# Optimization experiments

Measured on AMD Instinct MI355X. Metric: run time of the kernel, lower is better.

Reference implementation:

```python
import jax, jax.numpy as jnp
import numpy as np

IN_C, HID, N_NODES, WINDOW = 8, 64, 20000, 8
N_BIG = N_NODES * WINDOW          # 160000 supernodes (window-stacked graph)
E, E_DEC = 1_600_000, 500_000
EPS = 1e-5
DH = 2 * HID + IN_C + WINDOW - 1  # 143, decoder hidden size


def _gcn(x, row, col, ew, W, b, n):
    # GCNConv with self-loops + symmetric normalization (PyG semantics)
    loop = jnp.arange(n)
    r = jnp.concatenate([row, loop])
    c = jnp.concatenate([col, loop])
    w = jnp.concatenate([ew, jnp.ones((n,), ew.dtype)])
    deg = jax.ops.segment_sum(w, c, num_segments=n)
    dis = jnp.where(deg > 0, jax.lax.rsqrt(jnp.maximum(deg, EPS)), 0.0)
    norm = dis[r] * w * dis[c]
    h = x @ W                                  # [n, HID]
    agg = jax.ops.segment_sum(norm[:, None] * h[r], c, num_segments=n)
    return agg + b


def _bn(x, g, be):
    # BatchNorm1d, training-mode batch statistics (biased var)
    m = x.mean(0)
    v = x.var(0)
    return (x - m) * jax.lax.rsqrt(v + EPS) * g + be


def _lstm(X, Wih, Whh, bih, bhh):
    # X: [T, B, F]; PyTorch gate order i,f,g,o
    Hd = Whh.shape[1]
    B = X.shape[1]

    def step(carry, xt):
        h, c = carry
        gates = xt @ Wih.T + h @ Whh.T + bih + bhh
        i, f, g, o = jnp.split(gates, 4, axis=-1)
        c = jax.nn.sigmoid(f) * c + jax.nn.sigmoid(i) * jnp.tanh(g)
        h = jax.nn.sigmoid(o) * jnp.tanh(c)
        return (h, c), h

    init = (jnp.zeros((B, Hd), X.dtype), jnp.zeros((B, Hd), X.dtype))
    (h, _), ys = jax.lax.scan(step, init, X)
    return ys, h


def setup_inputs() -> dict:
    key = jax.random.key(0)
    ks = jax.random.split(key, 20)
    f32 = jnp.float32
    sc = lambda k, shape, fan: (jax.random.normal(k, shape, f32) / np.sqrt(fan)).astype(f32)
    d = {}
    d["x"] = jax.random.normal(ks[0], (N_BIG, IN_C), f32)
    d["edge_attr"] = jax.random.uniform(ks[1], (E,), f32)
    d["edge_index"] = jax.random.randint(ks[2], (2, E), 0, N_BIG)
    d["edge_weights_index"] = jax.random.randint(ks[3], (2, E_DEC), 0, N_NODES)
    # GCN layer 1 and 2
    d["W1"] = sc(ks[4], (IN_C, HID), IN_C); d["b1"] = jnp.zeros((HID,), f32)
    d["g1"] = jnp.ones((HID,), f32); d["be1"] = jnp.zeros((HID,), f32)
    d["W2"] = sc(ks[5], (HID, HID), HID); d["b2"] = jnp.zeros((HID,), f32)
    d["g2"] = jnp.ones((HID,), f32); d["be2"] = jnp.zeros((HID,), f32)
    # LSTM 1 (input 2*HID) and LSTM 2 (input HID)
    d["Wih1"] = sc(ks[6], (4 * HID, 2 * HID), 2 * HID)
    d["Whh1"] = sc(ks[7], (4 * HID, HID), HID)
    d["bih1"] = jnp.zeros((4 * HID,), f32); d["bhh1"] = jnp.zeros((4 * HID,), f32)
    d["Wih2"] = sc(ks[8], (4 * HID, HID), HID)
    d["Whh2"] = sc(ks[9], (4 * HID, HID), HID)
    d["bih2"] = jnp.zeros((4 * HID,), f32); d["bhh2"] = jnp.zeros((4 * HID,), f32)
    # Edge decoder MLP
    d["dWa"] = sc(ks[10], (2 * DH, DH), 2 * DH); d["dba"] = jnp.zeros((DH,), f32)
    d["dWb"] = sc(ks[11], (DH, 1), DH); d["dbb"] = jnp.zeros((1,), f32)
    return d


def reference(x, edge_attr, W1, b1, g1, be1, W2, b2, g2, be2,
              Wih1, Whh1, bih1, bhh1, Wih2, Whh2, bih2, bhh2,
              dWa, dba, dWb, dbb, edge_index, edge_weights_index):
    row, col = edge_index[0], edge_index[1]
    # skip features S: first timestep full features + last channel of later steps
    Sx = x.reshape(WINDOW, N_NODES, IN_C).transpose(1, 0, 2)   # [N, W, C]
    S = jnp.concatenate([Sx[:, 0, :], Sx[:, 1:, IN_C - 1]], axis=1)  # [N, C+W-1]
    # two GCN layers (relu -> batchnorm; dropout identity in eval)
    h1 = _bn(jax.nn.relu(_gcn(x, row, col, edge_attr, W1, b1, N_BIG)), g1, be1)
    h2 = _bn(jax.nn.relu(_gcn(h1, row, col, edge_attr, W2, b2, N_BIG)), g2, be2)
    Xc = jnp.concatenate([h1, h2], axis=1).reshape(WINDOW, N_NODES, 2 * HID)
    y1, H1 = _lstm(Xc, Wih1, Whh1, bih1, bhh1)
    _, H2 = _lstm(y1, Wih2, Whh2, bih2, bhh2)
    node_emb = jnp.concatenate([H1, H2, S], axis=1)  # [N_NODES, DH]
    # edge decoder: gather-concat-MLP
    src, trg = edge_weights_index[0], edge_weights_index[1]
    ee = jnp.concatenate([node_emb[src], node_emb[trg]], axis=1)  # [E_DEC, 2*DH]
    h = jax.nn.relu(ee @ dWa + dba)
    return (h @ dWb + dbb).reshape(-1)
```

## Files before the change

kernel.cpp:

```cpp
#include <hip/hip_runtime.h>
#include <hip/hip_bf16.h>

#define IN_C 8
#define HID 64
#define N_NODES 20000
#define WINDOW 8
#define N_BIG 160000
#define NE 1600000
#define E_DEC 500000
#define DHV 143
#define EPSV 1e-5f
#define CAP 32
#define OVF_CAP 4096
#define NER 168
#define QS 16384.0f
#define IQS (1.0f / 16384.0f)
#define NPART 8
#define PART_SZ (N_BIG / NPART)
#define NEB (NE / 256)

typedef __hip_bfloat16 bf;
typedef __attribute__((ext_vector_type(8))) short short8;
typedef __attribute__((ext_vector_type(4))) float float4_;

__device__ __forceinline__ float b2f(bf v) { return __bfloat162float(v); }
__device__ __forceinline__ bf f2b(float v) { return __float2bfloat16(v); }
__device__ __forceinline__ float bflo(unsigned int u) { return __uint_as_float(u << 16); }
__device__ __forceinline__ float bfhi(unsigned int u) { return __uint_as_float(u & 0xffff0000u); }
__device__ __forceinline__ unsigned int packbf2(float lo, float hi) {
    unsigned int ul = __bfloat16_as_ushort(f2b(lo));
    unsigned int uh = __bfloat16_as_ushort(f2b(hi));
    return ul | (uh << 16);
}
__device__ __forceinline__ float sigf(float x) {
    return __builtin_amdgcn_rcpf(1.f + __expf(-x));
}
__device__ __forceinline__ float tanhfast(float x) {
    x = fminf(fmaxf(x, -15.f), 15.f);
    float e = __expf(2.f * x);
    return (e - 1.f) * __builtin_amdgcn_rcpf(e + 1.f);
}

__global__ __launch_bounds__(256) void k_prepfill(
    const int* ei, const float* ea, int* cnt, unsigned int* bucket, int* ovfn, float4* ovf,
    const float* Wih2, const float* Whh2, const float* bih1, const float* bhh1,
    const float* bih2, const float* bhh2, const float* dWa,
    bf* B2f, float* bc1, float* bc2, bf* Bpqf)
{
    int tid = threadIdx.x;
    if (blockIdx.x < NPART * NEB) {
        int p = blockIdx.x & (NPART - 1);
        int chunk = blockIdx.x >> 3;
        int e = chunk * 256 + tid;
        int c = ei[NE + e];
        if (c >= p * PART_SZ && c < (p + 1) * PART_SZ) {
            int r = ei[e];
            float a = ea[e];
            unsigned int q = (unsigned int)(a * QS + 0.5f);
            if (q > 16383u) q = 16383u;
            int pp = atomicAdd(&cnt[c], 1);
            if (pp < CAP) bucket[(size_t)c * CAP + pp] = ((unsigned int)r << 14) | q;
            else {
                int qq = atomicAdd(ovfn, 1);
                if (qq < OVF_CAP) ovf[qq] = make_float4(__int_as_float(c), __int_as_float(r), a, 0.f);
            }
        }
        return;
    }
    int i0 = (blockIdx.x - NPART * NEB) * 256 + tid;
    int stride = 512 * 256;
    for (int i = i0; i < 16 * 4 * 64 * 8; i += stride) {
        int j = i & 7, lane = (i >> 3) & 63, r = i >> 9;
        int c = r & 3, ct = r >> 2;
        int q = lane >> 4, l15 = lane & 15;
        int n = ct * 16 + l15, k = c * 32 + q * 8 + j;
        B2f[i] = f2b((k < 64) ? Wih2[n * 64 + k] : Whh2[n * 64 + (k - 64)]);
    }
    for (int i = i0; i < 256; i += stride) {
        bc1[i] = bih1[i] + bhh1[i];
        bc2[i] = bih2[i] + bhh2[i];
    }
    for (int i = i0; i < 18 * 5 * 64 * 8; i += stride) {
        int j = i & 7, lane = (i >> 3) & 63, r = i >> 9;
        int c = r % 5, ct = r / 5;
        int q = lane >> 4, l15 = lane & 15;
        int n = ct * 16 + l15, k = c * 32 + q * 8 + j;
        float v = 0.f;
        if (k < DHV) {
            if (n < DHV) v = dWa[k * DHV + n];
            else if (n >= 144 && n < 144 + DHV) v = dWa[(DHV + k) * DHV + (n - 144)];
        }
        Bpqf[i] = f2b(v);
    }
}

__global__ __launch_bounds__(256) void k_xw1dis(const float* x, const float* W1,
        const int* cnt, const unsigned int* bucket, const int* ovfn, const float4* ovf,
        float* dis, bf* hbufb) {
    __shared__ float Ws[8][64];
    __shared__ float xs[8][8];
    int tid = threadIdx.x;
    Ws[tid >> 6][tid & 63] = W1[tid];
    Ws[4 + (tid >> 6)][tid & 63] = W1[256 + tid];
    int nb0 = blockIdx.x * 8;
    if (tid < 64) xs[tid >> 3][tid & 7] = x[nb0 * IN_C + tid];
    __syncthreads();
    int wv = tid >> 6, half = (tid >> 5) & 1, l = tid & 31;
    int nl = wv * 2 + half;
    int c = nb0 + nl;
    int n = cnt[c];
    int nbk = (n < CAP) ? n : CAP;
    float s = 0.f;
    for (int i = l; i < nbk; i += 32) s += (float)(bucket[(size_t)c * CAP + i] & 0x3FFFu);
    s *= IQS;
    if (n > CAP) {
        int m = *ovfn; if (m > OVF_CAP) m = OVF_CAP;
        for (int i = l; i < m; i += 32) {
            float4 v = ovf[i];
            if (__float_as_int(v.x) == c) s += v.z;
        }
    }
#pragma unroll
    for (int off = 16; off > 0; off >>= 1) s += __shfl_xor(s, off);
    float dv = rsqrtf(fmaxf(1.f + s, EPSV));
    if (l == 0) dis[c] = dv;
    float a0 = 0.f, a1 = 0.f;
#pragma unroll
    for (int k = 0; k < IN_C; k++) {
        float xv = xs[nl][k];
        a0 += xv * Ws[k][2 * l];
        a1 += xv * Ws[k][2 * l + 1];
    }
    *(unsigned int*)(hbufb + (size_t)c * 64 + 2 * l) = packbf2(dv * a0, dv * a1);
}

__global__ __launch_bounds__(256) void k_gcn_gather(const bf* h, const float* dis, const int* cnt,
                             const unsigned int* bucket, const int* ovfn, const float4* ovf,
                             const float* bias, bf* outb, float* part) {
    __shared__ float4 red[256];
    int tid = threadIdx.x;
    int wv = (blockIdx.x * 256 + tid) >> 6;
    int half = (tid >> 5) & 1, l = tid & 31;
    int c = wv * 2 + half;
    unsigned int hv = *(const unsigned int*)(h + (size_t)c * 64 + 2 * l);
    float ax = bflo(hv), ay = bfhi(hv);
    size_t o = (size_t)c * CAP;
    int nfull = cnt[c];
    int n = (nfull < CAP) ? nfull : CAP;
    int e = 0;
    for (; e + 8 <= n; e += 8) {
        unsigned int p[8];
#pragma unroll
        for (int j = 0; j < 8; j++) p[j] = bucket[o + e + j];
        unsigned int v[8];
#pragma unroll
        for (int j = 0; j < 8; j++)
            v[j] = *(const unsigned int*)(h + (size_t)(p[j] >> 14) * 64 + 2 * l);
#pragma unroll
        for (int j = 0; j < 8; j++) {
            float a = (float)(p[j] & 0x3FFFu) * IQS;
            ax += a * bflo(v[j]); ay += a * bfhi(v[j]);
        }
    }
    for (; e + 4 <= n; e += 4) {
        unsigned int p[4];
#pragma unroll
        for (int j = 0; j < 4; j++) p[j] = bucket[o + e + j];
        unsigned int v[4];
#pragma unroll
        for (int j = 0; j < 4; j++)
            v[j] = *(const unsigned int*)(h + (size_t)(p[j] >> 14) * 64 + 2 * l);
#pragma unroll
        for (int j = 0; j < 4; j++) {
            float a = (float)(p[j] & 0x3FFFu) * IQS;
            ax += a * bflo(v[j]); ay += a * bfhi(v[j]);
        }
    }
    for (; e < n; e++) {
        unsigned int p = bucket[o + e];
        unsigned int v = *(const unsigned int*)(h + (size_t)(p >> 14) * 64 + 2 * l);
        float a = (float)(p & 0x3FFFu) * IQS;
        ax += a * bflo(v);
        ay += a * bfhi(v);
    }
    if (nfull > CAP) {
        int m = *ovfn; if (m > OVF_CAP) m = OVF_CAP;
        for (int i = 0; i < m; i++) {
            float4 v = ovf[i];
            if (__float_as_int(v.x) == c) {
                unsigned int hw = *(const unsigned int*)(h + (size_t)__float_as_int(v.y) * 64 + 2 * l);
                ax += v.z * bflo(hw);
                ay += v.z * bfhi(hw);
            }
        }
    }
    float dv = dis[c];
    float2 bv = *(const float2*)(bias + 2 * l);
    float vx = fmaxf(dv * ax + bv.x, 0.f);
    float vy = fmaxf(dv * ay + bv.y, 0.f);
    *(unsigned int*)(outb + (size_t)c * 64 + 2 * l) = packbf2(vx, vy);
    red[tid] = make_float4(vx, vy, vx * vx, vy * vy);
    __syncthreads();
    if (tid < 32) {
        float4 s = make_float4(0.f, 0.f, 0.f, 0.f);
#pragma unroll
        for (int i = 0; i < 8; i++) {
            float4 v = red[((i >> 1) << 6) + ((i & 1) << 5) + tid];
            s.x += v.x; s.y += v.y; s.z += v.z; s.w += v.w;
        }
        float* pb = part + (size_t)blockIdx.x * 128;
        pb[2 * tid] = s.x; pb[2 * tid + 1] = s.y;
        pb[64 + 2 * tid] = s.z; pb[64 + 2 * tid + 1] = s.w;
    }
}

__global__ __launch_bounds__(256) void k_bnred(const float* part, int nblk, float* stats_out) {
    __shared__ float s[256];
    float acc = 0.f;
    for (int b = threadIdx.x; b < nblk; b += 256) acc += part[(size_t)b * 128 + blockIdx.x];
    s[threadIdx.x] = acc;
    __syncthreads();
    for (int off = 128; off; off >>= 1) {
        if (threadIdx.x < off) s[threadIdx.x] += s[threadIdx.x + off];
        __syncthreads();
    }
    if (threadIdx.x == 0) stats_out[blockIdx.x] = s[0];
}

__global__ __launch_bounds__(256) void k_fold1(const float* W2, const float* g1, const float* be1,
                                               const float* stats, bf* W2t, float* w2b, float* AC) {
    __shared__ float A[64], C[64];
    int tid = threadIdx.x;
    if (tid < 64) {
        float m = stats[tid] * (1.f / (float)N_BIG);
        float var = stats[64 + tid] * (1.f / (float)N_BIG) - m * m;
        float a = g1[tid] * rsqrtf(var + EPSV);
        float c = be1[tid] - m * a;
        A[tid] = a; C[tid] = c;
        AC[tid] = a; AC[64 + tid] = c;
    }
    __syncthreads();
    for (int i = tid; i < 4096; i += 256) {
        int n = i >> 6, k = i & 63;
        W2t[i] = f2b(W2[k * 64 + n] * A[k]);
    }
    if (tid < 64) {
        float s = 0.f;
        for (int k = 0; k < 64; k++) s += C[k] * W2[k * 64 + tid];
        w2b[tid] = s;
    }
}

__global__ void k_fold2(const float* Wih1, const float* Whh1,
                        const float* g2, const float* be2, const float* stats,
                        const float* AC, const float* bih1, const float* bhh1,
                        bf* B1f, float* bc1f) {
    int i0 = blockIdx.x * blockDim.x + threadIdx.x;
    int stride = gridDim.x * blockDim.x;
    for (int i = i0; i < 16 * 6 * 64 * 8; i += stride) {
        int j = i & 7, lane = (i >> 3) & 63, r = i >> 9;
        int c = r % 6, ct = r / 6;
        int q = lane >> 4, l15 = lane & 15;
        int n = ct * 16 + l15, k = c * 32 + q * 8 + j;
        float w = (k < 128) ? Wih1[n * 128 + k] : Whh1[n * 64 + (k - 128)];
        float scale = 1.f;
        if (k < 64) scale = AC[k];
        else if (k < 128) {
            int ch = k - 64;
            float m = stats[128 + ch] * (1.f / (float)N_BIG);
            float var = stats[192 + ch] * (1.f / (float)N_BIG) - m * m;
            scale = g2[ch] * rsqrtf(var + EPSV);
        }
        B1f[i] = f2b(w * scale);
    }
    for (int n = i0; n < 256; n += stride) {
        float s = bih1[n] + bhh1[n];
        for (int k = 0; k < 64; k++) s += AC[64 + k] * Wih1[n * 128 + k];
        for (int ch = 0; ch < 64; ch++) {
            float m = stats[128 + ch] * (1.f / (float)N_BIG);
            float var = stats[192 + ch] * (1.f / (float)N_BIG) - m * m;
            float a = g2[ch] * rsqrtf(var + EPSV);
            float c2v = be2[ch] - m * a;
            s += c2v * Wih1[n * 128 + 64 + ch];
        }
        bc1f[n] = s;
    }
}

__global__ __launch_bounds__(256) void k_h1w2(const bf* h1b, const bf* W2t, const float* w2b,
                                              const float* dis, bf* outb) {
    int tid = threadIdx.x, w = tid >> 6, lane = tid & 63;
    int q = lane >> 4, l15 = lane & 15;
    size_t r0 = (size_t)blockIdx.x * 64 + w * 16;
    float4_ acc[4];
#pragma unroll
    for (int ct = 0; ct < 4; ct++) acc[ct] = (float4_){0.f, 0.f, 0.f, 0.f};
#pragma unroll
    for (int c = 0; c < 2; c++) {
        int koff = c * 32 + q * 8;
        short8 a = *(const short8*)(h1b + (r0 + l15) * 64 + koff);
#pragma unroll
        for (int ct = 0; ct < 4; ct++) {
            short8 b = *(const short8*)(W2t + (size_t)(ct * 16 + l15) * 64 + koff);
            acc[ct] = __builtin_amdgcn_mfma_f32_16x16x32_bf16(a, b, acc[ct], 0, 0, 0);
        }
    }
    size_t node0 = r0 + q * 4;
#pragma unroll
    for (int reg = 0; reg < 4; reg++) {
        float dv = dis[node0 + reg];
#pragma unroll
        for (int ct = 0; ct < 4; ct++)
            outb[(node0 + reg) * 64 + ct * 16 + l15] = f2b(dv * (acc[ct][reg] + w2b[ct * 16 + l15]));
    }
}

__global__ __launch_bounds__(256, 1) void k_lstm_fused(
    const bf* h1b, const bf* h2b, const bf* B1f, const bf* B2f,
    const float* bc1, const float* bc2, bf* H1out, bf* H2out)
{
    __shared__ bf h1s[2][32][72];
    __shared__ bf h2s[2][32][72];
    int tid = threadIdx.x, w = tid >> 6, lane = tid & 63;
    int q = lane >> 4, l15 = lane & 15;
    int gnode0 = blockIdx.x * 32;
    short8 B1r[6][4];
    short8 B2r[4][4];
#pragma unroll
    for (int c = 0; c < 6; c++)
#pragma unroll
        for (int g = 0; g < 4; g++)
            B1r[c][g] = *(const short8*)(B1f + (size_t)(((w + 4 * g) * 6 + c) * 64 + lane) * 8);
#pragma unroll
    for (int c = 0; c < 4; c++)
#pragma unroll
        for (int g = 0; g < 4; g++)
            B2r[c][g] = *(const short8*)(B2f + (size_t)(((w + 4 * g) * 4 + c) * 64 + lane) * 8);
    float c1[2][4] = {}, c2[2][4] = {};
    float bv1[4], bv2[4];
#pragma unroll
    for (int g = 0; g < 4; g++) {
        bv1[g] = bc1[(w + 4 * g) * 16 + l15];
        bv2[g] = bc2[(w + 4 * g) * 16 + l15];
    }
    for (int t = 0; t < WINDOW; t++) {
        int cur = t & 1, prv = cur ^ 1;
        const size_t toff = (size_t)t * N_NODES * 64;
        float4_ acc[2][4];
#pragma unroll
        for (int m = 0; m < 2; m++)
#pragma unroll
            for (int g = 0; g < 4; g++) acc[m][g] = (float4_){bv1[g], bv1[g], bv1[g], bv1[g]};
#pragma unroll
        for (int c = 0; c < 4; c++) {
            const bf* sp = (c < 2) ? h1b + toff : h2b + toff;
            int koff = (c & 1) * 32 + q * 8;
#pragma unroll
            for (int m = 0; m < 2; m++) {
                short8 a = *(const short8*)(sp + (size_t)(gnode0 + m * 16 + l15) * 64 + koff);
#pragma unroll
                for (int g = 0; g < 4; g++)
                    acc[m][g] = __builtin_amdgcn_mfma_f32_16x16x32_bf16(a, B1r[c][g], acc[m][g], 0, 0, 0);
            }
        }
        if (t > 0) {
#pragma unroll
            for (int c = 4; c < 6; c++) {
                int koff = (c & 1) * 32 + q * 8;
#pragma unroll
                for (int m = 0; m < 2; m++) {
                    short8 a = *(const short8*)&h1s[prv][m * 16 + l15][koff];
#pragma unroll
                    for (int g = 0; g < 4; g++)
                        acc[m][g] = __builtin_amdgcn_mfma_f32_16x16x32_bf16(a, B1r[c][g], acc[m][g], 0, 0, 0);
                }
            }
        }
#pragma unroll
        for (int m = 0; m < 2; m++)
#pragma unroll
            for (int reg = 0; reg < 4; reg++) {
                float gi = acc[m][0][reg], gf = acc[m][1][reg];
                float gg = acc[m][2][reg], go = acc[m][3][reg];
                float co = (t == 0) ? 0.f : c1[m][reg];
                float cn = sigf(gf) * co + sigf(gi) * tanhfast(gg);
                float hn = sigf(go) * tanhfast(cn);
                c1[m][reg] = cn;
                int nl = m * 16 + q * 4 + reg;
                h1s[cur][nl][w * 16 + l15] = f2b(hn);
                if (t == WINDOW - 1)
                    H1out[(size_t)(gnode0 + nl) * 64 + w * 16 + l15] = f2b(hn);
            }
        __syncthreads();
#pragma unroll
        for (int m = 0; m < 2; m++)
#pragma unroll
            for (int g = 0; g < 4; g++) acc[m][g] = (float4_){bv2[g], bv2[g], bv2[g], bv2[g]};
#pragma unroll
        for (int c = 0; c < 2; c++) {
            int koff = (c & 1) * 32 + q * 8;
#pragma unroll
            for (int m = 0; m < 2; m++) {
                short8 a = *(const short8*)&h1s[cur][m * 16 + l15][koff];
#pragma unroll
                for (int g = 0; g < 4; g++)
                    acc[m][g] = __builtin_amdgcn_mfma_f32_16x16x32_bf16(a, B2r[c][g], acc[m][g], 0, 0, 0);
            }
        }
        if (t > 0) {
#pragma unroll
            for (int c = 2; c < 4; c++) {
                int koff = (c & 1) * 32 + q * 8;
#pragma unroll
                for (int m = 0; m < 2; m++) {
                    short8 a = *(const short8*)&h2s[prv][m * 16 + l15][koff];
#pragma unroll
                    for (int g = 0; g < 4; g++)
                        acc[m][g] = __builtin_amdgcn_mfma_f32_16x16x32_bf16(a, B2r[c][g], acc[m][g], 0, 0, 0);
                }
            }
        }
#pragma unroll
        for (int m = 0; m < 2; m++)
#pragma unroll
            for (int reg = 0; reg < 4; reg++) {
                float gi = acc[m][0][reg], gf = acc[m][1][reg];
                float gg = acc[m][2][reg], go = acc[m][3][reg];
                float co = (t == 0) ? 0.f : c2[m][reg];
                float cn = sigf(gf) * co + sigf(gi) * tanhfast(gg);
                float hn = sigf(go) * tanhfast(cn);
                c2[m][reg] = cn;
                int nl = m * 16 + q * 4 + reg;
                h2s[cur][nl][w * 16 + l15] = f2b(hn);
                if (t == WINDOW - 1)
                    H2out[(size_t)(gnode0 + nl) * 64 + w * 16 + l15] = f2b(hn);
            }
        __syncthreads();
    }
}

__global__ __launch_bounds__(256) void k_pq(const bf* H1, const bf* H2, const float* x,
                                            const bf* Bpqf, const float* dba, bf* PQb) {
    __shared__ bf ne[64][NER];
    int tid = threadIdx.x, w = tid >> 6, lane = tid & 63;
    int q = lane >> 4, l15 = lane & 15;
    int r0 = blockIdx.x * 64;
    for (int i = tid; i < 64 * 16; i += 256) {
        int rr = i >> 4, cc = (i & 15) * 4;
        int gr = r0 + rr;
        uint2 v1 = make_uint2(0u, 0u), v2 = make_uint2(0u, 0u);
        if (gr < N_NODES) {
            v1 = *(const uint2*)(H1 + (size_t)gr * 64 + cc);
            v2 = *(const uint2*)(H2 + (size_t)gr * 64 + cc);
        }
        *(uint2*)&ne[rr][cc] = v1;
        *(uint2*)&ne[rr][64 + cc] = v2;
    }
    for (int i = tid; i < 64 * 32; i += 256) {
        int rr = i >> 5, cc = 128 + (i & 31);
        int gr = r0 + rr;
        float v = 0.f;
        if (gr < N_NODES && cc < DHV) {
            int s = cc - 128;
            v = (s < 8) ? x[gr * IN_C + s] : x[(size_t)((s - 7) * N_NODES + gr) * IN_C + 7];
        }
        ne[rr][cc] = f2b(v);
    }
    __syncthreads();
    float4_ acc[18];
#pragma unroll
    for (int ct = 0; ct < 18; ct++) acc[ct] = (float4_){0.f, 0.f, 0.f, 0.f};
#pragma unroll
    for (int c = 0; c < 5; c++) {
        short8 a = *(const short8*)&ne[w * 16 + l15][c * 32 + q * 8];
#pragma unroll
        for (int ct = 0; ct < 18; ct++) {
            short8 b = *(const short8*)(Bpqf + (size_t)((ct * 5 + c) * 64 + lane) * 8);
            acc[ct] = __builtin_amdgcn_mfma_f32_16x16x32_bf16(a, b, acc[ct], 0, 0, 0);
        }
    }
#pragma unroll
    for (int reg = 0; reg < 4; reg++) {
        int nrow = r0 + w * 16 + q * 4 + reg;
        if (nrow < N_NODES)
#pragma unroll
            for (int ct = 0; ct < 18; ct++) {
                int col = ct * 16 + l15;
                float add = (ct < 9 && col < DHV) ? dba[col] : 0.f;
                PQb[(size_t)nrow * 288 + col] = f2b(acc[ct][reg] + add);
            }
    }
}

__global__ __launch_bounds__(256) void k_edge(const int* ewi, const bf* PQb,
                                              const float* dWb, const float* dbb, float* out) {
    int wv = (blockIdx.x * blockDim.x + threadIdx.x) >> 6;
    int half = (threadIdx.x >> 5) & 1, l = threadIdx.x & 31;
    int e = wv * 2 + half;
    if (e >= E_DEC) return;
    int src = ewi[e], trg = ewi[E_DEC + e];
    const bf* Pr = PQb + (size_t)src * 288;
    const bf* Qr = PQb + (size_t)trg * 288 + 144;
    float acc;
    {
        uint2 pv = *(const uint2*)(Pr + 4 * l);
        uint2 qv = *(const uint2*)(Qr + 4 * l);
        float4 wv4 = *(const float4*)(dWb + 4 * l);
        float s0 = fmaxf(bflo(pv.x) + bflo(qv.x), 0.f);
        float s1 = fmaxf(bfhi(pv.x) + bfhi(qv.x), 0.f);
        float s2 = fmaxf(bflo(pv.y) + bflo(qv.y), 0.f);
        float s3 = fmaxf(bfhi(pv.y) + bfhi(qv.y), 0.f);
        acc = s0 * wv4.x + s1 * wv4.y + s2 * wv4.z + s3 * wv4.w;
    }
    if (l < 4) {
        int u0 = 128 + 4 * l;
        uint2 pv = *(const uint2*)(Pr + u0);
        uint2 qv = *(const uint2*)(Qr + u0);
        float w0 = dWb[u0], w1 = dWb[u0 + 1], w2 = dWb[u0 + 2];
        float w3 = (u0 + 3 < DHV) ? dWb[u0 + 3] : 0.f;
        acc += fmaxf(bflo(pv.x) + bflo(qv.x), 0.f) * w0;
        acc += fmaxf(bfhi(pv.x) + bfhi(qv.x), 0.f) * w1;
        acc += fmaxf(bflo(pv.y) + bflo(qv.y), 0.f) * w2;
        acc += fmaxf(bfhi(pv.y) + bfhi(qv.y), 0.f) * w3;
    }
#pragma unroll
    for (int off = 16; off > 0; off >>= 1) acc += __shfl_xor(acc, off);
    if (l == 0) out[e] = acc + dbb[0];
}

extern "C" void kernel_launch(void* const* d_in, const int* in_sizes, int n_in,
                              void* d_out, int out_size, void* d_ws, size_t ws_size,
                              hipStream_t stream) {
    (void)in_sizes; (void)n_in; (void)out_size; (void)ws_size;
    const float* x    = (const float*)d_in[0];
    const float* ea   = (const float*)d_in[1];
    const int*   ei   = (const int*)d_in[2];
    const int*   ewi  = (const int*)d_in[3];
    const float* W1   = (const float*)d_in[4];
    const float* b1   = (const float*)d_in[5];
    const float* g1   = (const float*)d_in[6];
    const float* be1  = (const float*)d_in[7];
    const float* W2   = (const float*)d_in[8];
    const float* b2   = (const float*)d_in[9];
    const float* g2   = (const float*)d_in[10];
    const float* be2  = (const float*)d_in[11];
    const float* Wih1 = (const float*)d_in[12];
    const float* Whh1 = (const float*)d_in[13];
    const float* bih1 = (const float*)d_in[14];
    const float* bhh1 = (const float*)d_in[15];
    const float* Wih2 = (const float*)d_in[16];
    const float* Whh2 = (const float*)d_in[17];
    const float* bih2 = (const float*)d_in[18];
    const float* bhh2 = (const float*)d_in[19];
    const float* dWa  = (const float*)d_in[20];
    const float* dba  = (const float*)d_in[21];
    const float* dWb  = (const float*)d_in[22];
    const float* dbb  = (const float*)d_in[23];
    float* out = (float*)d_out;

    const size_t NSB = (size_t)N_BIG * 64;
    const size_t NS  = (size_t)N_NODES * 64;
    char* base = (char*)d_ws;
    size_t o = 0;
    float* dis  = (float*)(base + o); o += (size_t)N_BIG * 4;
    bf* PQb     = (bf*)(base + o);    o += NSB * 2;
    bf* hbufb   = (bf*)(base + o);    o += NSB * 2;
    bf* h1b     = (bf*)(base + o);    o += NSB * 2;
    bf* h2b     = (bf*)(base + o);    o += NSB * 2;
    bf* hs1     = (bf*)(base + o);    o += NS * 2;
    bf* hs2     = (bf*)(base + o);    o += NS * 2;
    bf* B1f     = (bf*)(base + o);    o += (size_t)16 * 6 * 64 * 8 * 2;
    bf* B2f     = (bf*)(base + o);    o += (size_t)16 * 4 * 64 * 8 * 2;
    bf* W2t     = (bf*)(base + o);    o += 64 * 64 * 2;
    bf* Bpqf    = (bf*)(base + o);    o += (size_t)18 * 5 * 64 * 8 * 2;
    float* bc1  = (float*)(base + o); o += 256 * 4;
    float* bc2  = (float*)(base + o); o += 256 * 4;
    float* stats= (float*)(base + o); o += 256 * 4;
    float* w2b  = (float*)(base + o); o += 64 * 4;
    float* AC   = (float*)(base + o); o += 128 * 4;
    float* bc1f = (float*)(base + o); o += 256 * 4;
    int* cnt    = (int*)(base + o);   o += (size_t)N_BIG * 4;
    int* ovfn   = (int*)(base + o);   o += 256 * 4;
    float4* ovf = (float4*)(base + o); o += (size_t)OVF_CAP * 16;
    unsigned int* bucket = (unsigned int*)(base + o); o += (size_t)N_BIG * CAP * 4;
    float* part = (float*)(base + o); o += (size_t)20000 * 128 * 4;

    hipMemsetAsync(cnt, 0, ((size_t)N_BIG + 256) * 4, stream);
    k_prepfill<<<NPART * NEB + 512, 256, 0, stream>>>(ei, ea, cnt, bucket, ovfn, ovf,
                                               Wih2, Whh2, bih1, bhh1, bih2, bhh2, dWa,
                                               B2f, bc1, bc2, Bpqf);
    k_xw1dis<<<N_BIG / 8, 256, 0, stream>>>(x, W1, cnt, bucket, ovfn, ovf, dis, hbufb);

    k_gcn_gather<<<N_BIG / 8, 256, 0, stream>>>(hbufb, dis, cnt, bucket, ovfn, ovf, b1, h1b, part);
    k_bnred<<<128, 256, 0, stream>>>(part, 20000, stats);
    k_fold1<<<1, 256, 0, stream>>>(W2, g1, be1, stats, W2t, w2b, AC);

    k_h1w2<<<2500, 256, 0, stream>>>(h1b, W2t, w2b, dis, hbufb);
    k_gcn_gather<<<N_BIG / 8, 256, 0, stream>>>(hbufb, dis, cnt, bucket, ovfn, ovf, b2, h2b, part);
    k_bnred<<<128, 256, 0, stream>>>(part, 20000, stats + 128);
    k_fold2<<<64, 256, 0, stream>>>(Wih1, Whh1, g2, be2, stats, AC, bih1, bhh1, B1f, bc1f);

    k_lstm_fused<<<625, 256, 0, stream>>>(h1b, h2b, B1f, B2f, bc1f, bc2, hs1, hs2);

    k_pq<<<313, 256, 0, stream>>>(hs1, hs2, x, Bpqf, dba, PQb);
    k_edge<<<E_DEC / 8, 256, 0, stream>>>(ewi, PQb, dWb, dbb, out);
}
```

Before: 578.7 us.

## Use XCD-aware persistent blocks with per-partition atomic work cursors for edge bucketing

Result: slower. 1.471 ms (+154.2%).

```diff
diff --git a/kernel.cpp b/kernel.cpp
--- a/kernel.cpp
+++ b/kernel.cpp
@@ -18,6 +18,8 @@
 #define NPART 8
 #define PART_SZ (N_BIG / NPART)
 #define NEB (NE / 256)
+#define NFILL 4096
+#define XCC_HWREG 6164
 
 typedef __hip_bfloat16 bf;
 typedef __attribute__((ext_vector_type(8))) short short8;
@@ -42,32 +44,44 @@
 }
 
 __global__ __launch_bounds__(256) void k_prepfill(
-    const int* ei, const float* ea, int* cnt, unsigned int* bucket, int* ovfn, float4* ovf,
+    const int* ei, const float* ea, int* cnt, unsigned int* bucket, int* ovfn, int* cursor,
+    float4* ovf,
     const float* Wih2, const float* Whh2, const float* bih1, const float* bhh1,
     const float* bih2, const float* bhh2, const float* dWa,
     bf* B2f, float* bc1, float* bc2, bf* Bpqf)
 {
     int tid = threadIdx.x;
-    if (blockIdx.x < NPART * NEB) {
-        int p = blockIdx.x & (NPART - 1);
-        int chunk = blockIdx.x >> 3;
-        int e = chunk * 256 + tid;
-        int c = ei[NE + e];
-        if (c >= p * PART_SZ && c < (p + 1) * PART_SZ) {
-            int r = ei[e];
-            float a = ea[e];
-            unsigned int q = (unsigned int)(a * QS + 0.5f);
-            if (q > 16383u) q = 16383u;
-            int pp = atomicAdd(&cnt[c], 1);
-            if (pp < CAP) bucket[(size_t)c * CAP + pp] = ((unsigned int)r << 14) | q;
-            else {
-                int qq = atomicAdd(ovfn, 1);
-                if (qq < OVF_CAP) ovf[qq] = make_float4(__int_as_float(c), __int_as_float(r), a, 0.f);
+    if (blockIdx.x < NFILL) {
+        __shared__ int chunk_s;
+        int xcd = (int)(__builtin_amdgcn_s_getreg(XCC_HWREG)) & (NPART - 1);
+        for (int pp = 0; pp < NPART; pp++) {
+            int p = (xcd + pp) & (NPART - 1);
+            int lo = p * PART_SZ, hi = lo + PART_SZ;
+            for (;;) {
+                if (tid == 0) chunk_s = atomicAdd(&cursor[p], 1);
+                __syncthreads();
+                int chunk = chunk_s;
+                __syncthreads();
+                if (chunk >= NEB) break;
+                int e = chunk * 256 + tid;
+                int c = ei[NE + e];
+                if (c >= lo && c < hi) {
+                    int r = ei[e];
+                    float a = ea[e];
+                    unsigned int q = (unsigned int)(a * QS + 0.5f);
+                    if (q > 16383u) q = 16383u;
+                    int ppos = atomicAdd(&cnt[c], 1);
+                    if (ppos < CAP) bucket[(size_t)c * CAP + ppos] = ((unsigned int)r << 14) | q;
+                    else {
+                        int qq = atomicAdd(ovfn, 1);
+                        if (qq < OVF_CAP) ovf[qq] = make_float4(__int_as_float(c), __int_as_float(r), a, 0.f);
+                    }
+                }
             }
         }
         return;
     }
-    int i0 = (blockIdx.x - NPART * NEB) * 256 + tid;
+    int i0 = (blockIdx.x - NFILL) * 256 + tid;
     int stride = 512 * 256;
     for (int i = i0; i < 16 * 4 * 64 * 8; i += stride) {
         int j = i & 7, lane = (i >> 3) & 63, r = i >> 9;
@@ -584,9 +598,10 @@
     float4* ovf = (float4*)(base + o); o += (size_t)OVF_CAP * 16;
     unsigned int* bucket = (unsigned int*)(base + o); o += (size_t)N_BIG * CAP * 4;
     float* part = (float*)(base + o); o += (size_t)20000 * 128 * 4;
+    int* cursor = ovfn + 8;
 
     hipMemsetAsync(cnt, 0, ((size_t)N_BIG + 256) * 4, stream);
-    k_prepfill<<<NPART * NEB + 512, 256, 0, stream>>>(ei, ea, cnt, bucket, ovfn, ovf,
+    k_prepfill<<<NFILL + 512, 256, 0, stream>>>(ei, ea, cnt, bucket, ovfn, cursor, ovf,
                                                Wih2, Whh2, bih1, bhh1, bih2, bhh2, dWa,
                                                B2f, bc1, bc2, Bpqf);
     k_xw1dis<<<N_BIG / 8, 256, 0, stream>>>(x, W1, cnt, bucket, ovfn, ovf, dis, hbufb);
```
